# Optimization experiments

Measured on AMD Instinct MI355X. Metric: run time of the kernel, lower is better.

The kernel has to match this reference:

```python
import jax, jax.numpy as jnp
import numpy as np

NEG_SLOPE = 0.2
HEADS = 4
HEAD_DIM = 32


def setup_inputs() -> dict:
    key = jax.random.key(0)
    ks = jax.random.split(key, 6)
    N, E, D_IN = 50000, 600000, 128
    x = jax.random.normal(ks[0], (N, D_IN), dtype=jnp.float32)
    edge_index = jax.random.randint(ks[1], (2, E), 0, N, dtype=jnp.int64)
    W = jax.random.normal(ks[2], (D_IN, HEADS * HEAD_DIM), dtype=jnp.float32) * (1.0 / np.sqrt(D_IN))
    att_src = jax.random.normal(ks[3], (HEADS, HEAD_DIM), dtype=jnp.float32) * 0.1
    att_dst = jax.random.normal(ks[4], (HEADS, HEAD_DIM), dtype=jnp.float32) * 0.1
    bias = jax.random.normal(ks[5], (HEADS * HEAD_DIM,), dtype=jnp.float32) * 0.01
    return {"x": x, "edge_index": edge_index, "W": W, "att_src": att_src, "att_dst": att_dst, "bias": bias}


def reference(x, edge_index, W, att_src, att_dst, bias):
    N = x.shape[0]
    # add self-loops (PyG GATConv default add_self_loops=True)
    loop = jnp.arange(N, dtype=edge_index.dtype)
    src = jnp.concatenate([edge_index[0], loop])  # [E+N]
    dst = jnp.concatenate([edge_index[1], loop])
    # linear projection -> [N, H, D]
    h = (x @ W).reshape(N, HEADS, HEAD_DIM)
    # per-node attention halves: [N, H]
    a_src = jnp.einsum('nhd,hd->nh', h, att_src)
    a_dst = jnp.einsum('nhd,hd->nh', h, att_dst)
    # per-edge logits + leaky relu
    logits = a_src[src] + a_dst[dst]  # [E', H]
    logits = jnp.where(logits >= 0, logits, NEG_SLOPE * logits)
    # softmax over edges grouped by destination node
    m = jax.ops.segment_max(logits, dst, num_segments=N)  # [N, H]
    ealpha = jnp.exp(logits - m[dst])
    denom = jax.ops.segment_sum(ealpha, dst, num_segments=N)
    alpha = ealpha / denom[dst]  # every node has a self-loop -> denom > 0
    # weighted message aggregation: scatter-add h[src] * alpha -> dst
    msgs = h[src] * alpha[:, :, None]  # [E', H, D]
    out = jax.ops.segment_sum(msgs, dst, num_segments=N)  # [N, H, D]
    out = out.reshape(N, HEADS * HEAD_DIM) + bias
    return jnp.tanh(out)
```

## Files before the change

kernel.cpp:

```cpp
#include <hip/hip_runtime.h>
#include <hip/hip_bf16.h>
#include <math.h>

#define NEG_SLOPE 0.2f
#define DMODEL 128
#define CAP 96
#define POISON 0xAAAAAAAAu
#define NPREP 65

typedef __attribute__((ext_vector_type(8))) short short8;
typedef __attribute__((ext_vector_type(4))) float floatx4;

__device__ __forceinline__ float leaky(float x) { return x >= 0.f ? x : NEG_SLOPE * x; }
__device__ __forceinline__ float b2f(short v) {
    return __uint_as_float(((unsigned)(unsigned short)v) << 16);
}
__device__ __forceinline__ float fast_tanh(float x) {
    return 1.f - 2.f / (__expf(2.f * x) + 1.f);
}

__global__ __launch_bounds__(256) void kpcb(
    const float* __restrict__ W, const float* __restrict__ att_src,
    const float* __restrict__ att_dst, const int* __restrict__ srcs,
    const int* __restrict__ dsts, __hip_bfloat16* __restrict__ Wt,
    __hip_bfloat16* __restrict__ Wat, unsigned* __restrict__ deg,
    int* __restrict__ bucket, int E)
{
    if ((int)blockIdx.x < NPREP) {
        int idx = blockIdx.x * 256 + threadIdx.x;
        if (idx < DMODEL * DMODEL) {
            int n = idx >> 7, k = idx & 127;
            Wt[idx] = __float2bfloat16(W[k * DMODEL + n]);
        }
        if (idx < 16 * DMODEL) {
            int col = idx >> 7, k = idx & 127;
            float v = 0.f;
            if (col < 8) {
                int hd = col & 3;
                const float* att = (col < 4) ? att_src : att_dst;
                #pragma unroll 8
                for (int d = 0; d < 32; d++)
                    v += W[k * DMODEL + hd * 32 + d] * att[hd * 32 + d];
            }
            Wat[idx] = __float2bfloat16(v);
        }
        return;
    }
    int i = ((blockIdx.x - NPREP) * 256 + threadIdx.x) * 4;
    if (i + 4 <= E) {
        int4 s = *(const int4*)(srcs + i);
        int4 d = *(const int4*)(dsts + i);
        int r0 = (int)(atomicAdd(&deg[d.x], 1u) - POISON);
        int r1 = (int)(atomicAdd(&deg[d.y], 1u) - POISON);
        int r2 = (int)(atomicAdd(&deg[d.z], 1u) - POISON);
        int r3 = (int)(atomicAdd(&deg[d.w], 1u) - POISON);
        bucket[(size_t)d.x * CAP + r0] = s.x;
        bucket[(size_t)d.y * CAP + r1] = s.y;
        bucket[(size_t)d.z * CAP + r2] = s.z;
        bucket[(size_t)d.w * CAP + r3] = s.w;
    } else if (i < E) {
        for (int e = i; e < E; e++) {
            int r = (int)(atomicAdd(&deg[dsts[e]], 1u) - POISON);
            bucket[(size_t)dsts[e] * CAP + r] = srcs[e];
        }
    }
}

__global__ __launch_bounds__(256) void k1m(const float* __restrict__ x,
                                           const __hip_bfloat16* __restrict__ Wt,
                                           const __hip_bfloat16* __restrict__ Wat,
                                           __hip_bfloat16* __restrict__ h,
                                           float* __restrict__ a_src,
                                           float* __restrict__ a_dst, int N) {
    const int wv = threadIdx.x >> 6, lane = threadIdx.x & 63;
    const int node0 = blockIdx.x * 64 + wv * 16;
    const int m = lane & 15, kq = lane >> 4;
    floatx4 acc[9];
    #pragma unroll
    for (int t = 0; t < 9; t++) acc[t] = (floatx4)(0.f);

    int arow = node0 + m; if (arow >= N) arow = N - 1;
    const float* ap = x + (size_t)arow * DMODEL + kq * 8;
    const short* bp = (const short*)Wt + m * DMODEL + kq * 8;
    const short* wp = (const short*)Wat + m * DMODEL + kq * 8;

    #pragma unroll
    for (int ks = 0; ks < 4; ks++) {
        float4 a0 = *(const float4*)(ap + ks * 32);
        float4 a1 = *(const float4*)(ap + ks * 32 + 4);
        __hip_bfloat16 ab[8] = {
            __float2bfloat16(a0.x), __float2bfloat16(a0.y),
            __float2bfloat16(a0.z), __float2bfloat16(a0.w),
            __float2bfloat16(a1.x), __float2bfloat16(a1.y),
            __float2bfloat16(a1.z), __float2bfloat16(a1.w)};
        short8 a = *(const short8*)ab;
        #pragma unroll
        for (int nt = 0; nt < 8; nt++) {
            short8 b = *(const short8*)(bp + nt * 16 * DMODEL + ks * 32);
            acc[nt] = __builtin_amdgcn_mfma_f32_16x16x32_bf16(a, b, acc[nt], 0, 0, 0);
        }
        short8 b8 = *(const short8*)(wp + ks * 32);
        acc[8] = __builtin_amdgcn_mfma_f32_16x16x32_bf16(a, b8, acc[8], 0, 0, 0);
    }

    #pragma unroll
    for (int nt = 0; nt < 8; nt++) {
        #pragma unroll
        for (int r = 0; r < 4; r++) {
            int node = node0 + kq * 4 + r;
            if (node < N)
                h[(size_t)node * DMODEL + nt * 16 + m] = __float2bfloat16(acc[nt][r]);
        }
    }
    if (m < 8) {
        #pragma unroll
        for (int r = 0; r < 4; r++) {
            int node = node0 + kq * 4 + r;
            if (node < N) {
                if (m < 4) a_src[(size_t)node * 4 + m] = acc[8][r];
                else       a_dst[(size_t)node * 4 + (m - 4)] = acc[8][r];
            }
        }
    }
}

__global__ __launch_bounds__(256) void kagg(
    const unsigned* __restrict__ deg, const int* __restrict__ bucket,
    const __hip_bfloat16* __restrict__ h, const float* __restrict__ a_src,
    const float* __restrict__ a_dst, const float* __restrict__ bias,
    float* __restrict__ out, int N)
{
    __shared__ float2 pid[8][32][4];
    const int hw = threadIdx.x >> 5;
    const int l = threadIdx.x & 31;
    const int head = l >> 3;
    const int node = blockIdx.x * 8 + hw;
    if (node >= N) return;

    const float4 adw = *(const float4*)(a_dst + (size_t)node * 4);
    const float4 asw = *(const float4*)(a_src + (size_t)node * 4);
    float4 ls;
    ls.x = leaky(asw.x + adw.x); ls.y = leaky(asw.y + adw.y);
    ls.z = leaky(asw.z + adw.z); ls.w = leaky(asw.w + adw.w);

    float4 denom4 = {0.f, 0.f, 0.f, 0.f};
    short4 hs = *(const short4*)(h + (size_t)node * DMODEL + l * 4);
    float4 acc = {b2f(hs.x), b2f(hs.y), b2f(hs.z), b2f(hs.w)};

    const int dcount = (int)(deg[node] - POISON);
    const int j0 = node * CAP, j1 = j0 + dcount;
    for (int base = j0; base < j1; base += 32) {
        int idx = base + l;
        bool valid = idx < j1;
        int sv = valid ? bucket[idx] : 0;
        float4 a4 = *(const float4*)(a_src + (size_t)sv * 4);
        float4 p4;
        p4.x = valid ? __expf(leaky(a4.x + adw.x) - ls.x) : 0.f;
        p4.y = valid ? __expf(leaky(a4.y + adw.y) - ls.y) : 0.f;
        p4.z = valid ? __expf(leaky(a4.z + adw.z) - ls.z) : 0.f;
        p4.w = valid ? __expf(leaky(a4.w + adw.w) - ls.w) : 0.f;
        denom4.x += p4.x; denom4.y += p4.y; denom4.z += p4.z; denom4.w += p4.w;
        float idf = __int_as_float(sv);
        float4 w0 = {p4.x, idf, p4.y, idf};
        float4 w1 = {p4.z, idf, p4.w, idf};
        *(float4*)&pid[hw][l][0] = w0;
        *(float4*)&pid[hw][l][2] = w1;
        int cnt = j1 - base; if (cnt > 32) cnt = 32;
        int rounded = (cnt + 3) & ~3;
        for (int jj = 0; jj < rounded; jj += 4) {
            float2 pi0 = pid[hw][jj + 0][head];
            float2 pi1 = pid[hw][jj + 1][head];
            float2 pi2 = pid[hw][jj + 2][head];
            float2 pi3 = pid[hw][jj + 3][head];
            int s0 = __float_as_int(pi0.y), s1 = __float_as_int(pi1.y);
            int s2 = __float_as_int(pi2.y), s3 = __float_as_int(pi3.y);
            short4 g0 = *(const short4*)(h + (size_t)s0 * DMODEL + l * 4);
            short4 g1 = *(const short4*)(h + (size_t)s1 * DMODEL + l * 4);
            short4 g2 = *(const short4*)(h + (size_t)s2 * DMODEL + l * 4);
            short4 g3 = *(const short4*)(h + (size_t)s3 * DMODEL + l * 4);
            acc.x += pi0.x * b2f(g0.x) + pi1.x * b2f(g1.x)
                   + pi2.x * b2f(g2.x) + pi3.x * b2f(g3.x);
            acc.y += pi0.x * b2f(g0.y) + pi1.x * b2f(g1.y)
                   + pi2.x * b2f(g2.y) + pi3.x * b2f(g3.y);
            acc.z += pi0.x * b2f(g0.z) + pi1.x * b2f(g1.z)
                   + pi2.x * b2f(g2.z) + pi3.x * b2f(g3.z);
            acc.w += pi0.x * b2f(g0.w) + pi1.x * b2f(g1.w)
                   + pi2.x * b2f(g2.w) + pi3.x * b2f(g3.w);
        }
    }
    #pragma unroll
    for (int off = 1; off < 32; off <<= 1) {
        denom4.x += __shfl_xor(denom4.x, off, 64);
        denom4.y += __shfl_xor(denom4.y, off, 64);
        denom4.z += __shfl_xor(denom4.z, off, 64);
        denom4.w += __shfl_xor(denom4.w, off, 64);
    }
    float denom = 1.f + ((head == 0) ? denom4.x : (head == 1) ? denom4.y
                        : (head == 2) ? denom4.z : denom4.w);

    float4 b = *(const float4*)(bias + l * 4);
    float inv = 1.f / denom;
    float4 o;
    o.x = fast_tanh(acc.x * inv + b.x);
    o.y = fast_tanh(acc.y * inv + b.y);
    o.z = fast_tanh(acc.z * inv + b.z);
    o.w = fast_tanh(acc.w * inv + b.w);
    *(float4*)(out + (size_t)node * DMODEL + l * 4) = o;
}

extern "C" void kernel_launch(void* const* d_in, const int* in_sizes, int n_in,
                              void* d_out, int out_size, void* d_ws, size_t ws_size,
                              hipStream_t stream) {
    const float* x       = (const float*)d_in[0];
    const int*   edges   = (const int*)d_in[1];
    const float* W       = (const float*)d_in[2];
    const float* att_src = (const float*)d_in[3];
    const float* att_dst = (const float*)d_in[4];
    const float* bias    = (const float*)d_in[5];
    float* out = (float*)d_out;

    const int N = in_sizes[0] / DMODEL;
    const int E = in_sizes[1] / 2;
    const int* srcs = edges;
    const int* dsts = edges + E;

    __hip_bfloat16* Wt  = (__hip_bfloat16*)d_ws;
    __hip_bfloat16* Wat = Wt + DMODEL * DMODEL;
    __hip_bfloat16* h   = Wat + 16 * DMODEL;
    float* a_src_d = (float*)(h + (size_t)N * DMODEL);
    float* a_dst_d = a_src_d + (size_t)N * 4;
    unsigned* deg = (unsigned*)(a_dst_d + (size_t)N * 4);
    int* bucket   = (int*)(deg + N);

    const int nkcb = (E / 4 + 255) / 256;
    kpcb<<<NPREP + nkcb, 256, 0, stream>>>(W, att_src, att_dst, srcs, dsts,
                                           Wt, Wat, deg, bucket, E);
    k1m<<<(N + 63) / 64, 256, 0, stream>>>(x, Wt, Wat, h, a_src_d, a_dst_d, N);
    kagg<<<(N + 7) / 8, 256, 0, stream>>>(deg, bucket, h, a_src_d, a_dst_d,
                                          bias, out, N);
}
```

Measured before the change: 164.1 us.

## Merge edge bucketing with projection GEMM into one kernel launch

Weight preparation (transpose to bf16 plus the attention-folded columns) moves into a small standalone kernel. The edge bucketing atomics are fused with the x@W projection MFMA kernel, with blocks split by index. The memory- and atomic-heavy bucketing can then overlap with the compute-bound GEMM instead of running in separate launches. The risk is that the GEMM blocks are scheduled after the bucketing blocks and gain little concurrency, while the extra prep launch adds a serial step.

```diff
diff --git a/kernel.cpp b/kernel.cpp
--- a/kernel.cpp
+++ b/kernel.cpp
@@ -6,7 +6,6 @@
 #define DMODEL 128
 #define CAP 96
 #define POISON 0xAAAAAAAAu
-#define NPREP 65
 
 typedef __attribute__((ext_vector_type(8))) short short8;
 typedef __attribute__((ext_vector_type(4))) float floatx4;
@@ -19,61 +18,61 @@
     return 1.f - 2.f / (__expf(2.f * x) + 1.f);
 }
 
-__global__ __launch_bounds__(256) void kpcb(
+__global__ __launch_bounds__(256) void kprep(
     const float* __restrict__ W, const float* __restrict__ att_src,
-    const float* __restrict__ att_dst, const int* __restrict__ srcs,
-    const int* __restrict__ dsts, __hip_bfloat16* __restrict__ Wt,
-    __hip_bfloat16* __restrict__ Wat, unsigned* __restrict__ deg,
-    int* __restrict__ bucket, int E)
+    const float* __restrict__ att_dst, __hip_bfloat16* __restrict__ Wt,
+    __hip_bfloat16* __restrict__ Wat)
 {
-    if ((int)blockIdx.x < NPREP) {
-        int idx = blockIdx.x * 256 + threadIdx.x;
-        if (idx < DMODEL * DMODEL) {
-            int n = idx >> 7, k = idx & 127;
-            Wt[idx] = __float2bfloat16(W[k * DMODEL + n]);
-        }
-        if (idx < 16 * DMODEL) {
-            int col = idx >> 7, k = idx & 127;
-            float v = 0.f;
-            if (col < 8) {
-                int hd = col & 3;
-                const float* att = (col < 4) ? att_src : att_dst;
-                #pragma unroll 8
-                for (int d = 0; d < 32; d++)
-                    v += W[k * DMODEL + hd * 32 + d] * att[hd * 32 + d];
+    int idx = blockIdx.x * 256 + threadIdx.x;
+    if (idx < DMODEL * DMODEL) {
+        int n = idx >> 7, k = idx & 127;
+        Wt[idx] = __float2bfloat16(W[k * DMODEL + n]);
+    }
+    if (idx < 16 * DMODEL) {
+        int col = idx >> 7, k = idx & 127;
+        float v = 0.f;
+        if (col < 8) {
+            int hd = col & 3;
+            const float* att = (col < 4) ? att_src : att_dst;
+            #pragma unroll 8
+            for (int d = 0; d < 32; d++)
+                v += W[k * DMODEL + hd * 32 + d] * att[hd * 32 + d];
+        }
+        Wat[idx] = __float2bfloat16(v);
+    }
+}
+
+__global__ __launch_bounds__(256) void kmerge(
+    const float* __restrict__ x, const __hip_bfloat16* __restrict__ Wt,
+    const __hip_bfloat16* __restrict__ Wat, const int* __restrict__ srcs,
+    const int* __restrict__ dsts, __hip_bfloat16* __restrict__ h,
+    float* __restrict__ a_src, float* __restrict__ a_dst,
+    unsigned* __restrict__ deg, int* __restrict__ bucket,
+    int E, int N, int nkcb)
+{
+    if ((int)blockIdx.x < nkcb) {
+        int i = (blockIdx.x * 256 + threadIdx.x) * 4;
+        if (i + 4 <= E) {
+            int4 s = *(const int4*)(srcs + i);
+            int4 d = *(const int4*)(dsts + i);
+            int r0 = (int)(atomicAdd(&deg[d.x], 1u) - POISON);
+            int r1 = (int)(atomicAdd(&deg[d.y], 1u) - POISON);
+            int r2 = (int)(atomicAdd(&deg[d.z], 1u) - POISON);
+            int r3 = (int)(atomicAdd(&deg[d.w], 1u) - POISON);
+            bucket[(size_t)d.x * CAP + r0] = s.x;
+            bucket[(size_t)d.y * CAP + r1] = s.y;
+            bucket[(size_t)d.z * CAP + r2] = s.z;
+            bucket[(size_t)d.w * CAP + r3] = s.w;
+        } else if (i < E) {
+            for (int e = i; e < E; e++) {
+                int r = (int)(atomicAdd(&deg[dsts[e]], 1u) - POISON);
+                bucket[(size_t)dsts[e] * CAP + r] = srcs[e];
             }
-            Wat[idx] = __float2bfloat16(v);
         }
         return;
     }
-    int i = ((blockIdx.x - NPREP) * 256 + threadIdx.x) * 4;
-    if (i + 4 <= E) {
-        int4 s = *(const int4*)(srcs + i);
-        int4 d = *(const int4*)(dsts + i);
-        int r0 = (int)(atomicAdd(&deg[d.x], 1u) - POISON);
-        int r1 = (int)(atomicAdd(&deg[d.y], 1u) - POISON);
-        int r2 = (int)(atomicAdd(&deg[d.z], 1u) - POISON);
-        int r3 = (int)(atomicAdd(&deg[d.w], 1u) - POISON);
-        bucket[(size_t)d.x * CAP + r0] = s.x;
-        bucket[(size_t)d.y * CAP + r1] = s.y;
-        bucket[(size_t)d.z * CAP + r2] = s.z;
-        bucket[(size_t)d.w * CAP + r3] = s.w;
-    } else if (i < E) {
-        for (int e = i; e < E; e++) {
-            int r = (int)(atomicAdd(&deg[dsts[e]], 1u) - POISON);
-            bucket[(size_t)dsts[e] * CAP + r] = srcs[e];
-        }
-    }
-}
-
-__global__ __launch_bounds__(256) void k1m(const float* __restrict__ x,
-                                           const __hip_bfloat16* __restrict__ Wt,
-                                           const __hip_bfloat16* __restrict__ Wat,
-                                           __hip_bfloat16* __restrict__ h,
-                                           float* __restrict__ a_src,
-                                           float* __restrict__ a_dst, int N) {
     const int wv = threadIdx.x >> 6, lane = threadIdx.x & 63;
-    const int node0 = blockIdx.x * 64 + wv * 16;
+    const int node0 = ((int)blockIdx.x - nkcb) * 64 + wv * 16;
     const int m = lane & 15, kq = lane >> 4;
     floatx4 acc[9];
     #pragma unroll
@@ -233,9 +232,12 @@
     int* bucket   = (int*)(deg + N);
 
     const int nkcb = (E / 4 + 255) / 256;
-    kpcb<<<NPREP + nkcb, 256, 0, stream>>>(W, att_src, att_dst, srcs, dsts,
-                                           Wt, Wat, deg, bucket, E);
-    k1m<<<(N + 63) / 64, 256, 0, stream>>>(x, Wt, Wat, h, a_src_d, a_dst_d, N);
+    const int nmm  = (N + 63) / 64;
+
+    kprep<<<65, 256, 0, stream>>>(W, att_src, att_dst, Wt, Wat);
+    kmerge<<<nkcb + nmm, 256, 0, stream>>>(x, Wt, Wat, srcs, dsts, h,
+                                           a_src_d, a_dst_d, deg, bucket,
+                                           E, N, nkcb);
     kagg<<<(N + 7) / 8, 256, 0, stream>>>(deg, bucket, h, a_src_d, a_dst_d,
                                           bias, out, N);
 }
```

New measurement: 160.9 us. About the same (-2.0%).
